# Optimization experiments

Hardware: AMD Instinct MI355X
Metric: run time of the kernel (lower is better)

## Reference

```python
import jax, jax.numpy as jnp
import numpy as np

D = 2048
N_SLOTS = 8
ALPHA_MIN = 0.02
FAST_DECAY = 0.95
ALPHA_BOOST = 1.0
B = 16384


def setup_inputs() -> dict:
    key = jax.random.key(0)
    ks = jax.random.split(key, 12)
    h = jax.random.normal(ks[0], (B, D), dtype=jnp.float32)
    neighbor_msg = jax.random.normal(ks[1], (B, D), dtype=jnp.float32)
    keys = jax.random.normal(ks[2], (N_SLOTS, D), dtype=jnp.float32) / (D ** 0.5)
    # torch nn.Linear convention: W [out, in], y = x @ W.T + b
    Wr = jax.random.normal(ks[3], (D, D), dtype=jnp.float32) * 0.02
    br = jnp.zeros((D,), dtype=jnp.float32)
    Wc = jax.random.normal(ks[4], (2, 2 * D), dtype=jnp.float32) * 0.02
    bc = jnp.zeros((2,), dtype=jnp.float32)
    Ww = jax.random.normal(ks[5], (D, 2 * D), dtype=jnp.float32) * 0.02
    bw = jnp.zeros((D,), dtype=jnp.float32)
    state = jax.random.normal(ks[6], (N_SLOTS, D), dtype=jnp.float32) * 0.1
    fast = jax.random.normal(ks[7], (N_SLOTS, D), dtype=jnp.float32) * 0.1
    return {"h": h, "neighbor_msg": neighbor_msg, "keys": keys,
            "Wr": Wr, "br": br, "Wc": Wc, "bc": bc, "Ww": Ww, "bw": bw,
            "state": state, "fast": fast}


def reference(h, neighbor_msg, keys, Wr, br, Wc, bc, Ww, bw, state, fast):
    # read_proj
    q = h @ Wr.T + br                                  # [B, D]
    attn = jax.nn.softmax(q @ keys.T, axis=-1)         # [B, n_slots]
    read = attn @ (state + fast)                       # [B, D]
    # ctrl -> add/erase gates (erase computed but unused downstream, as in source)
    ctrl = jnp.concatenate([h, read], axis=-1) @ Wc.T + bc   # [B, 2]
    add = jax.nn.sigmoid(ctrl[:, 0:1])
    erase = jax.nn.sigmoid(ctrl[:, 1:2])
    alpha = jnp.clip(ALPHA_MIN + (1.0 - ALPHA_MIN) * jnp.mean(add), 0.0, 1.0)
    alpha = jnp.clip(alpha * ALPHA_BOOST, 0.0, 1.0)
    # attention-weighted write into slots
    w_in = jnp.concatenate([h + neighbor_msg, read], axis=-1)  # [B, 2D]
    delta = attn.T @ (w_in @ Ww.T + bw)                # [n_slots, D]
    new_state = (1.0 - alpha) * state + alpha * delta
    new_fast = FAST_DECAY * fast + (1.0 - FAST_DECAY) * delta
    return read, attn, alpha, new_state, new_fast
```

## Files before the change

### kernel.cpp

```cpp
#include <hip/hip_runtime.h>
#include <math.h>

#define D 2048
#define NS 8
#define BTOT 16384

#define ATTN_OFF  ((size_t)BTOT * D)
#define ALPHA_OFF (ATTN_OFF + (size_t)BTOT * NS)
#define STATE_OFF (ALPHA_OFF + 1)
#define FAST_OFF  (STATE_OFF + (size_t)NS * D)

#define WS_SM    0
#define WS_KPX   16384
#define WS_GS    34816
#define WS_PB    51200
#define WS_LB    215040
#define WS_SWC   215048
#define WS_GALL  215056

__global__ void __launch_bounds__(256) kZ(const float* __restrict__ st, const float* __restrict__ fa,
                                          const float* __restrict__ Wc, float* __restrict__ ws) {
  int i = blockIdx.x * 256 + threadIdx.x;
  if (i < 16384) {
    ws[WS_SM + i] = st[i] + fa[i];
  } else if (i < 32768) {
    ws[WS_KPX + (i - 16384)] = 0.f;
  } else if (i < 34816) {
    ws[WS_KPX + 16384 + (i - 32768)] = Wc[i - 32768];
  } else if (i < 51200) {
    ws[WS_GS + (i - 34816)] = 0.f;
  } else if (i < 67584) {
    ws[WS_PB + (i - 51200)] = 0.f;
  } else if (i < 67680) {
    ws[WS_LB + (i - 67584)] = 0.f;
  }
}

__global__ void __launch_bounds__(256) kA(const float* __restrict__ keys,
                                          const float* __restrict__ Wr,
                                          float* __restrict__ kpx) {
  int e = blockIdx.x * 256 + threadIdx.x;
  int d0 = blockIdx.y * 64;
  float acc[NS] = {0.f,0.f,0.f,0.f,0.f,0.f,0.f,0.f};
  for (int d = d0; d < d0 + 64; ++d) {
    float wv = Wr[(size_t)d * D + e];
#pragma unroll
    for (int s = 0; s < NS; ++s) acc[s] += keys[s * D + d] * wv;
  }
#pragma unroll
  for (int s = 0; s < NS; ++s) atomicAdd(&kpx[s * D + e], acc[s]);
}

__global__ void __launch_bounds__(256) kC(const float* __restrict__ keys,
                                          const float* __restrict__ br,
                                          const float* __restrict__ Wc,
                                          const float* __restrict__ sm,
                                          float* __restrict__ lb, float* __restrict__ swc) {
  int t = threadIdx.x;
  int idx = blockIdx.x * 256 + t;
  float brv = br[idx];
  float wcr = Wc[D + idx];
  float v[16];
#pragma unroll
  for (int s = 0; s < NS; ++s) {
    v[s]     = keys[s * D + idx] * brv;
    v[8 + s] = sm[s * D + idx] * wcr;
  }
#pragma unroll
  for (int off = 32; off > 0; off >>= 1) {
#pragma unroll
    for (int k = 0; k < 16; ++k) v[k] += __shfl_down(v[k], off);
  }
  __shared__ float red[4 * 16];
  int lane = t & 63, wid = t >> 6;
  if (lane == 0) {
#pragma unroll
    for (int k = 0; k < 16; ++k) red[wid * 16 + k] = v[k];
  }
  __syncthreads();
  if (t < 16) {
    float tot = red[t] + red[16 + t] + red[32 + t] + red[48 + t];
    if (t < 8) atomicAdd(&lb[t], tot); else atomicAdd(&swc[t - 8], tot);
  }
}

__global__ void __launch_bounds__(256) k1aF(const float* __restrict__ h,
                                            const float* __restrict__ kpx,
                                            const float* __restrict__ lb, const float* __restrict__ swc,
                                            const float* __restrict__ bc,
                                            float* __restrict__ attn, float* __restrict__ gall) {
  __shared__ float4 kl[9 * 512];
  __shared__ float red2[4 * 9];
  int t = threadIdx.x;
  const float4* kp4 = (const float4*)kpx;
  for (int i = t; i < 4608; i += 256) kl[i] = kp4[i];
  __syncthreads();

  int w = t >> 6, lane = t & 63;
  int row0 = blockIdx.x * 32 + w * 8;
  float lbv[8], swv[8];
#pragma unroll
  for (int s = 0; s < NS; ++s) { lbv[s] = lb[s]; swv[s] = swc[s]; }
  float bc0 = bc[0];
  float cs[9] = {0.f,0.f,0.f,0.f,0.f,0.f,0.f,0.f,0.f};

  for (int r = 0; r < 8; ++r) {
    int row = row0 + r;
    const float4* h4 = (const float4*)h + (size_t)row * 512;
    float4 hv[8];
#pragma unroll
    for (int j = 0; j < 8; ++j) hv[j] = h4[lane + 64 * j];
    float acc[9] = {0.f,0.f,0.f,0.f,0.f,0.f,0.f,0.f,0.f};
#pragma unroll
    for (int j = 0; j < 8; ++j) {
#pragma unroll
      for (int s = 0; s < 9; ++s) {
        float4 kv = kl[s * 512 + lane + 64 * j];
        acc[s] += hv[j].x * kv.x + hv[j].y * kv.y + hv[j].z * kv.z + hv[j].w * kv.w;
      }
    }
#pragma unroll
    for (int off = 32; off > 0; off >>= 1) {
#pragma unroll
      for (int s = 0; s < 9; ++s) acc[s] += __shfl_xor(acc[s], off);
    }
    float lg[8]; float m = -1e30f;
#pragma unroll
    for (int s = 0; s < NS; ++s) { lg[s] = acc[s] + lbv[s]; m = fmaxf(m, lg[s]); }
    float sum = 0.f;
#pragma unroll
    for (int s = 0; s < NS; ++s) { lg[s] = expf(lg[s] - m); sum += lg[s]; }
    float inv = 1.f / sum;
    float x = acc[8] + bc0;
#pragma unroll
    for (int s = 0; s < NS; ++s) { lg[s] *= inv; x += lg[s] * swv[s]; cs[s] += lg[s]; }
    float add = 1.f / (1.f + expf(-x));
    cs[8] += add;
    if (lane == 0) {
      float4* ao = (float4*)(attn + (size_t)row * NS);
      ao[0] = make_float4(lg[0], lg[1], lg[2], lg[3]);
      ao[1] = make_float4(lg[4], lg[5], lg[6], lg[7]);
    }
  }
  if (lane == 0) {
#pragma unroll
    for (int k = 0; k < 9; ++k) red2[w * 9 + k] = cs[k];
  }
  __syncthreads();
  if (t < 9) {
    float tot = red2[t] + red2[9 + t] + red2[18 + t] + red2[27 + t];
    atomicAdd(&gall[64 + t], tot);
  }
}

static __device__ __forceinline__ float4 f4fma(float s, float4 a, float4 c) {
  c.x += s * a.x; c.y += s * a.y; c.z += s * a.z; c.w += s * a.w; return c;
}

__global__ void __launch_bounds__(256, 3) k2n(const float* __restrict__ h, const float* __restrict__ nm,
                                              const float* __restrict__ sm, const float* __restrict__ attn,
                                              float* __restrict__ readout, float* __restrict__ pb,
                                              float* __restrict__ gsb) {
  __shared__ float4 lp[4][NS][64];
  int t = threadIdx.x;
  int c4 = t & 63, r4 = t >> 6;
  int chunk = blockIdx.x, rc = blockIdx.y;
  int fbase = chunk * 64 + c4;
  const float4* sm4 = (const float4*)sm;
  float4 S[NS];
#pragma unroll
  for (int s = 0; s < NS; ++s) S[s] = sm4[s * 512 + fbase];
  float4 P[NS], Q[NS];
#pragma unroll
  for (int s = 0; s < NS; ++s) { P[s] = make_float4(0.f,0.f,0.f,0.f); Q[s] = make_float4(0.f,0.f,0.f,0.f); }
  int rowbase = rc * 128;
  for (int it = 0; it < 32; ++it) {
    int row = rowbase + it * 4 + r4;
    float4 hv = ((const float4*)h)[(size_t)row * 512 + fbase];
    float4 nv = ((const float4*)nm)[(size_t)row * 512 + fbase];
    const float* ar = attn + (size_t)row * NS;
    float a[NS];
#pragma unroll
    for (int s = 0; s < NS; ++s) a[s] = ar[s];
    float4 wv = make_float4(hv.x + nv.x, hv.y + nv.y, hv.z + nv.z, hv.w + nv.w);
    float4 rd = make_float4(0.f, 0.f, 0.f, 0.f);
#pragma unroll
    for (int s = 0; s < NS; ++s) {
      rd = f4fma(a[s], S[s], rd);
      P[s] = f4fma(a[s], wv, P[s]);
    }
#pragma unroll
    for (int s = 0; s < NS; ++s) Q[s] = f4fma(a[s], rd, Q[s]);
    ((float4*)readout)[(size_t)row * 512 + fbase] = rd;
  }
#pragma unroll
  for (int s = 0; s < NS; ++s) lp[r4][s][c4] = P[s];
  __syncthreads();
  for (int k = t; k < 512; k += 256) {
    int s = k >> 6, c = k & 63;
    float4 a0 = lp[0][s][c], b0 = lp[1][s][c], c0 = lp[2][s][c], d0 = lp[3][s][c];
    float4 v = make_float4(a0.x + b0.x + c0.x + d0.x, a0.y + b0.y + c0.y + d0.y,
                           a0.z + b0.z + c0.z + d0.z, a0.w + b0.w + c0.w + d0.w);
    float* dst = pb + s * D + chunk * 256 + c * 4;
    atomicAdd(dst + 0, v.x); atomicAdd(dst + 1, v.y);
    atomicAdd(dst + 2, v.z); atomicAdd(dst + 3, v.w);
  }
  __syncthreads();
#pragma unroll
  for (int s = 0; s < NS; ++s) lp[r4][s][c4] = Q[s];
  __syncthreads();
  for (int k = t; k < 512; k += 256) {
    int s = k >> 6, c = k & 63;
    float4 a0 = lp[0][s][c], b0 = lp[1][s][c], c0 = lp[2][s][c], d0 = lp[3][s][c];
    float4 v = make_float4(a0.x + b0.x + c0.x + d0.x, a0.y + b0.y + c0.y + d0.y,
                           a0.z + b0.z + c0.z + d0.z, a0.w + b0.w + c0.w + d0.w);
    float* dst = gsb + s * D + chunk * 256 + c * 4;
    atomicAdd(dst + 0, v.x); atomicAdd(dst + 1, v.y);
    atomicAdd(dst + 2, v.z); atomicAdd(dst + 3, v.w);
  }
}

__global__ void __launch_bounds__(256) k4(const float* __restrict__ Ww, const float* __restrict__ bw,
                                          const float* __restrict__ st, const float* __restrict__ fa,
                                          const float* __restrict__ p, const float* __restrict__ gs,
                                          const float* __restrict__ gall,
                                          float* __restrict__ outst, float* __restrict__ outfa,
                                          float* __restrict__ alphaout) {
  int dd = blockIdx.x, t = threadIdx.x;
  const float4* wr = (const float4*)(Ww + (size_t)dd * (2 * D));
  float4 w0 = wr[t], w1 = wr[256 + t], w2 = wr[512 + t], w3 = wr[768 + t];
  const float4* p4 = (const float4*)p;
  const float4* g4 = (const float4*)gs;
  float acc[NS];
#pragma unroll
  for (int s = 0; s < NS; ++s) {
    float4 pa = p4[s * 512 + t], pb2 = p4[s * 512 + 256 + t];
    float4 ga = g4[s * 512 + t], gb = g4[s * 512 + 256 + t];
    acc[s] = w0.x * pa.x + w0.y * pa.y + w0.z * pa.z + w0.w * pa.w
           + w1.x * pb2.x + w1.y * pb2.y + w1.z * pb2.z + w1.w * pb2.w
           + w2.x * ga.x + w2.y * ga.y + w2.z * ga.z + w2.w * ga.w
           + w3.x * gb.x + w3.y * gb.y + w3.z * gb.z + w3.w * gb.w;
  }
#pragma unroll
  for (int off = 32; off > 0; off >>= 1) {
#pragma unroll
    for (int v = 0; v < NS; ++v) acc[v] += __shfl_down(acc[v], off);
  }
  __shared__ float red[32];
  int lane = t & 63, wid = t >> 6;
  if (lane == 0) {
#pragma unroll
    for (int v = 0; v < NS; ++v) red[wid * 8 + v] = acc[v];
  }
  __syncthreads();
  if (t < NS) {
    float tot = red[t] + red[8 + t] + red[16 + t] + red[24 + t];
    float delta = tot + gall[64 + t] * bw[dd];
    float al = 0.02f + 0.98f * (gall[72] * (1.f / (float)BTOT));
    al = fminf(fmaxf(al, 0.f), 1.f);
    size_t idx = (size_t)t * D + dd;
    outst[idx] = (1.f - al) * st[idx] + al * delta;
    outfa[idx] = 0.95f * fa[idx] + 0.05f * delta;
  }
  if (dd == 0 && t == 0) {
    float al = 0.02f + 0.98f * (gall[72] * (1.f / (float)BTOT));
    alphaout[0] = fminf(fmaxf(al, 0.f), 1.f);
  }
}

extern "C" void kernel_launch(void* const* d_in, const int* in_sizes, int n_in,
                              void* d_out, int out_size, void* d_ws, size_t ws_size,
                              hipStream_t stream) {
  const float* h    = (const float*)d_in[0];
  const float* nm   = (const float*)d_in[1];
  const float* keys = (const float*)d_in[2];
  const float* Wr   = (const float*)d_in[3];
  const float* br   = (const float*)d_in[4];
  const float* Wc   = (const float*)d_in[5];
  const float* bc   = (const float*)d_in[6];
  const float* Ww   = (const float*)d_in[7];
  const float* bw   = (const float*)d_in[8];
  const float* st   = (const float*)d_in[9];
  const float* fa   = (const float*)d_in[10];
  float* out = (float*)d_out;
  float* ws  = (float*)d_ws;

  float* sm   = ws + WS_SM;
  float* kpx  = ws + WS_KPX;
  float* gsb  = ws + WS_GS;
  float* pb   = ws + WS_PB;
  float* lb   = ws + WS_LB;
  float* swc  = ws + WS_SWC;
  float* gall = ws + WS_GALL;
  float* attn = out + ATTN_OFF;

  kZ<<<265, 256, 0, stream>>>(st, fa, Wc, ws);
  kA<<<dim3(8, 32), 256, 0, stream>>>(keys, Wr, kpx);
  kC<<<8, 256, 0, stream>>>(keys, br, Wc, sm, lb, swc);
  k1aF<<<512, 256, 0, stream>>>(h, kpx, lb, swc, bc, attn, gall);
  k2n<<<dim3(8, 128), 256, 0, stream>>>(h, nm, sm, attn, out, pb, gsb);
  k4<<<2048, 256, 0, stream>>>(Ww, bw, st, fa, pb, gsb, gall, out + STATE_OFF, out + FAST_OFF,
                               out + ALPHA_OFF);
}
```

Before: 503.1 us.

## Replace attn^T·read accumulation with attention Gram matrix times slot memory

Since read = attn @ sm, the term attn^T @ read equals (attn^T attn) @ sm. The change drops the Q accumulation and second atomic pass in k2n and instead accumulates the 8x8 Gram matrix (36 upper entries) in the attention kernel. k4 then multiplies the Ww read-half against sm and combines with the Gram matrix. The attention kernel is also rewritten to use 16 threads per row reading kpx from global/L2 instead of LDS, and k2n is retiled to 32 columns by 8 row groups. This removes register pressure and half the atomics in k2n, at the cost of a 45-value shuffle reduction per row in k1r.

Result: faster. 444.5 us (-11.6%).

```diff
diff --git a/kernel.cpp b/kernel.cpp
--- a/kernel.cpp
+++ b/kernel.cpp
@@ -12,11 +12,10 @@
 
 #define WS_SM    0
 #define WS_KPX   16384
-#define WS_GS    34816
-#define WS_PB    51200
-#define WS_LB    215040
-#define WS_SWC   215048
-#define WS_GALL  215056
+#define WS_PB    34816
+#define WS_LB    51200
+#define WS_SWC   51208
+#define WS_GALL  51216
 
 __global__ void __launch_bounds__(256) kZ(const float* __restrict__ st, const float* __restrict__ fa,
                                           const float* __restrict__ Wc, float* __restrict__ ws) {
@@ -28,11 +27,9 @@
   } else if (i < 34816) {
     ws[WS_KPX + 16384 + (i - 32768)] = Wc[i - 32768];
   } else if (i < 51200) {
-    ws[WS_GS + (i - 34816)] = 0.f;
-  } else if (i < 67584) {
-    ws[WS_PB + (i - 51200)] = 0.f;
-  } else if (i < 67680) {
-    ws[WS_LB + (i - 67584)] = 0.f;
+    ws[WS_PB + (i - 34816)] = 0.f;
+  } else if (i < 51264) {
+    ws[WS_LB + (i - 51200)] = 0.f;
   }
 }
 
@@ -84,72 +81,70 @@
   }
 }
 
-__global__ void __launch_bounds__(256) k1aF(const float* __restrict__ h,
-                                            const float* __restrict__ kpx,
-                                            const float* __restrict__ lb, const float* __restrict__ swc,
-                                            const float* __restrict__ bc,
-                                            float* __restrict__ attn, float* __restrict__ gall) {
-  __shared__ float4 kl[9 * 512];
-  __shared__ float red2[4 * 9];
+__global__ void __launch_bounds__(256, 4) k1r(const float* __restrict__ h,
+                                              const float* __restrict__ kpx,
+                                              const float* __restrict__ lb, const float* __restrict__ swc,
+                                              const float* __restrict__ bc,
+                                              float* __restrict__ attn, float* __restrict__ gall) {
   int t = threadIdx.x;
+  int q = t & 15;
+  int row = blockIdx.x * 16 + (t >> 4);
+  const float4* h4 = (const float4*)h + (size_t)row * 512;
   const float4* kp4 = (const float4*)kpx;
-  for (int i = t; i < 4608; i += 256) kl[i] = kp4[i];
-  __syncthreads();
-
-  int w = t >> 6, lane = t & 63;
-  int row0 = blockIdx.x * 32 + w * 8;
-  float lbv[8], swv[8];
-#pragma unroll
-  for (int s = 0; s < NS; ++s) { lbv[s] = lb[s]; swv[s] = swc[s]; }
-  float bc0 = bc[0];
-  float cs[9] = {0.f,0.f,0.f,0.f,0.f,0.f,0.f,0.f,0.f};
-
-  for (int r = 0; r < 8; ++r) {
-    int row = row0 + r;
-    const float4* h4 = (const float4*)h + (size_t)row * 512;
-    float4 hv[8];
-#pragma unroll
-    for (int j = 0; j < 8; ++j) hv[j] = h4[lane + 64 * j];
-    float acc[9] = {0.f,0.f,0.f,0.f,0.f,0.f,0.f,0.f,0.f};
-#pragma unroll
-    for (int j = 0; j < 8; ++j) {
-#pragma unroll
-      for (int s = 0; s < 9; ++s) {
-        float4 kv = kl[s * 512 + lane + 64 * j];
-        acc[s] += hv[j].x * kv.x + hv[j].y * kv.y + hv[j].z * kv.z + hv[j].w * kv.w;
-      }
-    }
-#pragma unroll
-    for (int off = 32; off > 0; off >>= 1) {
-#pragma unroll
-      for (int s = 0; s < 9; ++s) acc[s] += __shfl_xor(acc[s], off);
-    }
-    float lg[8]; float m = -1e30f;
-#pragma unroll
-    for (int s = 0; s < NS; ++s) { lg[s] = acc[s] + lbv[s]; m = fmaxf(m, lg[s]); }
-    float sum = 0.f;
-#pragma unroll
-    for (int s = 0; s < NS; ++s) { lg[s] = expf(lg[s] - m); sum += lg[s]; }
-    float inv = 1.f / sum;
-    float x = acc[8] + bc0;
-#pragma unroll
-    for (int s = 0; s < NS; ++s) { lg[s] *= inv; x += lg[s] * swv[s]; cs[s] += lg[s]; }
-    float add = 1.f / (1.f + expf(-x));
-    cs[8] += add;
-    if (lane == 0) {
-      float4* ao = (float4*)(attn + (size_t)row * NS);
-      ao[0] = make_float4(lg[0], lg[1], lg[2], lg[3]);
-      ao[1] = make_float4(lg[4], lg[5], lg[6], lg[7]);
-    }
-  }
+  float acc[9] = {0.f,0.f,0.f,0.f,0.f,0.f,0.f,0.f,0.f};
+#pragma unroll 4
+  for (int j = 0; j < 32; ++j) {
+    float4 hv = h4[j * 16 + q];
+#pragma unroll
+    for (int s = 0; s < 9; ++s) {
+      float4 kv = kp4[s * 512 + j * 16 + q];
+      acc[s] += hv.x * kv.x + hv.y * kv.y + hv.z * kv.z + hv.w * kv.w;
+    }
+  }
+#pragma unroll
+  for (int off = 1; off <= 8; off <<= 1) {
+#pragma unroll
+    for (int s = 0; s < 9; ++s) acc[s] += __shfl_xor(acc[s], off);
+  }
+  float lg[8]; float m = -1e30f;
+#pragma unroll
+  for (int s = 0; s < NS; ++s) { lg[s] = acc[s] + lb[s]; m = fmaxf(m, lg[s]); }
+  float sum = 0.f;
+#pragma unroll
+  for (int s = 0; s < NS; ++s) { lg[s] = expf(lg[s] - m); sum += lg[s]; }
+  float inv = 1.f / sum;
+  float x = acc[8] + bc[0];
+#pragma unroll
+  for (int s = 0; s < NS; ++s) { lg[s] *= inv; x += lg[s] * swc[s]; }
+  float add = 1.f / (1.f + expf(-x));
+  if (q == 0) ((float4*)(attn + (size_t)row * NS))[0] = make_float4(lg[0], lg[1], lg[2], lg[3]);
+  if (q == 1) ((float4*)(attn + (size_t)row * NS))[1] = make_float4(lg[4], lg[5], lg[6], lg[7]);
+  float v[45];
+  {
+    int c = 0;
+#pragma unroll
+    for (int i = 0; i < NS; ++i)
+#pragma unroll
+      for (int j = i; j < NS; ++j) v[c++] = lg[i] * lg[j];
+  }
+#pragma unroll
+  for (int s = 0; s < NS; ++s) v[36 + s] = lg[s];
+  v[44] = add;
+#pragma unroll
+  for (int off = 16; off <= 32; off <<= 1) {
+#pragma unroll
+    for (int k = 0; k < 45; ++k) v[k] += __shfl_xor(v[k], off);
+  }
+  __shared__ float red[4][45];
+  int lane = t & 63, w = t >> 6;
   if (lane == 0) {
 #pragma unroll
-    for (int k = 0; k < 9; ++k) red2[w * 9 + k] = cs[k];
-  }
-  __syncthreads();
-  if (t < 9) {
-    float tot = red2[t] + red2[9 + t] + red2[18 + t] + red2[27 + t];
-    atomicAdd(&gall[64 + t], tot);
+    for (int k = 0; k < 45; ++k) red[w][k] = v[k];
+  }
+  __syncthreads();
+  if (t < 45) {
+    float tot = red[0][t] + red[1][t] + red[2][t] + red[3][t];
+    atomicAdd(&gall[t], tot);
   }
 }
 
@@ -157,25 +152,25 @@
   c.x += s * a.x; c.y += s * a.y; c.z += s * a.z; c.w += s * a.w; return c;
 }
 
-__global__ void __launch_bounds__(256, 3) k2n(const float* __restrict__ h, const float* __restrict__ nm,
+__global__ void __launch_bounds__(256, 4) k2n(const float* __restrict__ h, const float* __restrict__ nm,
                                               const float* __restrict__ sm, const float* __restrict__ attn,
-                                              float* __restrict__ readout, float* __restrict__ pb,
-                                              float* __restrict__ gsb) {
-  __shared__ float4 lp[4][NS][64];
+                                              float* __restrict__ readout, float* __restrict__ pb) {
+  __shared__ float4 lp[8][NS][32];
   int t = threadIdx.x;
-  int c4 = t & 63, r4 = t >> 6;
+  int c4 = t & 31, r4 = t >> 5;
   int chunk = blockIdx.x, rc = blockIdx.y;
-  int fbase = chunk * 64 + c4;
+  int fbase = chunk * 32 + c4;
   const float4* sm4 = (const float4*)sm;
   float4 S[NS];
 #pragma unroll
   for (int s = 0; s < NS; ++s) S[s] = sm4[s * 512 + fbase];
-  float4 P[NS], Q[NS];
-#pragma unroll
-  for (int s = 0; s < NS; ++s) { P[s] = make_float4(0.f,0.f,0.f,0.f); Q[s] = make_float4(0.f,0.f,0.f,0.f); }
-  int rowbase = rc * 128;
+  float4 P[NS];
+#pragma unroll
+  for (int s = 0; s < NS; ++s) P[s] = make_float4(0.f, 0.f, 0.f, 0.f);
+  int rowbase = rc * 256;
+#pragma unroll 2
   for (int it = 0; it < 32; ++it) {
-    int row = rowbase + it * 4 + r4;
+    int row = rowbase + it * 8 + r4;
     float4 hv = ((const float4*)h)[(size_t)row * 512 + fbase];
     float4 nv = ((const float4*)nm)[(size_t)row * 512 + fbase];
     const float* ar = attn + (size_t)row * NS;
@@ -189,40 +184,28 @@
       rd = f4fma(a[s], S[s], rd);
       P[s] = f4fma(a[s], wv, P[s]);
     }
-#pragma unroll
-    for (int s = 0; s < NS; ++s) Q[s] = f4fma(a[s], rd, Q[s]);
     ((float4*)readout)[(size_t)row * 512 + fbase] = rd;
   }
 #pragma unroll
   for (int s = 0; s < NS; ++s) lp[r4][s][c4] = P[s];
   __syncthreads();
-  for (int k = t; k < 512; k += 256) {
-    int s = k >> 6, c = k & 63;
-    float4 a0 = lp[0][s][c], b0 = lp[1][s][c], c0 = lp[2][s][c], d0 = lp[3][s][c];
-    float4 v = make_float4(a0.x + b0.x + c0.x + d0.x, a0.y + b0.y + c0.y + d0.y,
-                           a0.z + b0.z + c0.z + d0.z, a0.w + b0.w + c0.w + d0.w);
-    float* dst = pb + s * D + chunk * 256 + c * 4;
+  {
+    int s = t >> 5, c = t & 31;
+    float4 v = make_float4(0.f, 0.f, 0.f, 0.f);
+#pragma unroll
+    for (int g = 0; g < 8; ++g) {
+      float4 u = lp[g][s][c];
+      v.x += u.x; v.y += u.y; v.z += u.z; v.w += u.w;
+    }
+    float* dst = pb + s * D + chunk * 128 + c * 4;
     atomicAdd(dst + 0, v.x); atomicAdd(dst + 1, v.y);
     atomicAdd(dst + 2, v.z); atomicAdd(dst + 3, v.w);
   }
-  __syncthreads();
-#pragma unroll
-  for (int s = 0; s < NS; ++s) lp[r4][s][c4] = Q[s];
-  __syncthreads();
-  for (int k = t; k < 512; k += 256) {
-    int s = k >> 6, c = k & 63;
-    float4 a0 = lp[0][s][c], b0 = lp[1][s][c], c0 = lp[2][s][c], d0 = lp[3][s][c];
-    float4 v = make_float4(a0.x + b0.x + c0.x + d0.x, a0.y + b0.y + c0.y + d0.y,
-                           a0.z + b0.z + c0.z + d0.z, a0.w + b0.w + c0.w + d0.w);
-    float* dst = gsb + s * D + chunk * 256 + c * 4;
-    atomicAdd(dst + 0, v.x); atomicAdd(dst + 1, v.y);
-    atomicAdd(dst + 2, v.z); atomicAdd(dst + 3, v.w);
-  }
 }
 
 __global__ void __launch_bounds__(256) k4(const float* __restrict__ Ww, const float* __restrict__ bw,
                                           const float* __restrict__ st, const float* __restrict__ fa,
-                                          const float* __restrict__ p, const float* __restrict__ gs,
+                                          const float* __restrict__ p, const float* __restrict__ sm,
                                           const float* __restrict__ gall,
                                           float* __restrict__ outst, float* __restrict__ outfa,
                                           float* __restrict__ alphaout) {
@@ -230,40 +213,50 @@
   const float4* wr = (const float4*)(Ww + (size_t)dd * (2 * D));
   float4 w0 = wr[t], w1 = wr[256 + t], w2 = wr[512 + t], w3 = wr[768 + t];
   const float4* p4 = (const float4*)p;
-  const float4* g4 = (const float4*)gs;
-  float acc[NS];
+  const float4* s4 = (const float4*)sm;
+  float acc[16];
 #pragma unroll
   for (int s = 0; s < NS; ++s) {
     float4 pa = p4[s * 512 + t], pb2 = p4[s * 512 + 256 + t];
-    float4 ga = g4[s * 512 + t], gb = g4[s * 512 + 256 + t];
+    float4 sa = s4[s * 512 + t], sb = s4[s * 512 + 256 + t];
     acc[s] = w0.x * pa.x + w0.y * pa.y + w0.z * pa.z + w0.w * pa.w
-           + w1.x * pb2.x + w1.y * pb2.y + w1.z * pb2.z + w1.w * pb2.w
-           + w2.x * ga.x + w2.y * ga.y + w2.z * ga.z + w2.w * ga.w
-           + w3.x * gb.x + w3.y * gb.y + w3.z * gb.z + w3.w * gb.w;
+           + w1.x * pb2.x + w1.y * pb2.y + w1.z * pb2.z + w1.w * pb2.w;
+    acc[8 + s] = w2.x * sa.x + w2.y * sa.y + w2.z * sa.z + w2.w * sa.w
+               + w3.x * sb.x + w3.y * sb.y + w3.z * sb.z + w3.w * sb.w;
   }
 #pragma unroll
   for (int off = 32; off > 0; off >>= 1) {
 #pragma unroll
-    for (int v = 0; v < NS; ++v) acc[v] += __shfl_down(acc[v], off);
-  }
-  __shared__ float red[32];
+    for (int k = 0; k < 16; ++k) acc[k] += __shfl_down(acc[k], off);
+  }
+  __shared__ float red[4][16];
+  __shared__ float red2[16];
   int lane = t & 63, wid = t >> 6;
   if (lane == 0) {
 #pragma unroll
-    for (int v = 0; v < NS; ++v) red[wid * 8 + v] = acc[v];
-  }
+    for (int k = 0; k < 16; ++k) red[wid][k] = acc[k];
+  }
+  __syncthreads();
+  if (t < 16) red2[t] = red[0][t] + red[1][t] + red[2][t] + red[3][t];
   __syncthreads();
   if (t < NS) {
-    float tot = red[t] + red[8 + t] + red[16 + t] + red[24 + t];
-    float delta = tot + gall[64 + t] * bw[dd];
-    float al = 0.02f + 0.98f * (gall[72] * (1.f / (float)BTOT));
+    float delta = red2[t];
+#pragma unroll
+    for (int sp = 0; sp < NS; ++sp) {
+      int i = t < sp ? t : sp;
+      int j = t < sp ? sp : t;
+      int idx = i * 8 - (i * (i - 1)) / 2 + (j - i);
+      delta += gall[idx] * red2[8 + sp];
+    }
+    delta += gall[36 + t] * bw[dd];
+    float al = 0.02f + 0.98f * (gall[44] * (1.f / (float)BTOT));
     al = fminf(fmaxf(al, 0.f), 1.f);
-    size_t idx = (size_t)t * D + dd;
-    outst[idx] = (1.f - al) * st[idx] + al * delta;
-    outfa[idx] = 0.95f * fa[idx] + 0.05f * delta;
+    size_t idx2 = (size_t)t * D + dd;
+    outst[idx2] = (1.f - al) * st[idx2] + al * delta;
+    outfa[idx2] = 0.95f * fa[idx2] + 0.05f * delta;
   }
   if (dd == 0 && t == 0) {
-    float al = 0.02f + 0.98f * (gall[72] * (1.f / (float)BTOT));
+    float al = 0.02f + 0.98f * (gall[44] * (1.f / (float)BTOT));
     alphaout[0] = fminf(fmaxf(al, 0.f), 1.f);
   }
 }
@@ -287,18 +280,17 @@
 
   float* sm   = ws + WS_SM;
   float* kpx  = ws + WS_KPX;
-  float* gsb  = ws + WS_GS;
   float* pb   = ws + WS_PB;
   float* lb   = ws + WS_LB;
   float* swc  = ws + WS_SWC;
   float* gall = ws + WS_GALL;
   float* attn = out + ATTN_OFF;
 
-  kZ<<<265, 256, 0, stream>>>(st, fa, Wc, ws);
+  kZ<<<201, 256, 0, stream>>>(st, fa, Wc, ws);
   kA<<<dim3(8, 32), 256, 0, stream>>>(keys, Wr, kpx);
   kC<<<8, 256, 0, stream>>>(keys, br, Wc, sm, lb, swc);
-  k1aF<<<512, 256, 0, stream>>>(h, kpx, lb, swc, bc, attn, gall);
-  k2n<<<dim3(8, 128), 256, 0, stream>>>(h, nm, sm, attn, out, pb, gsb);
-  k4<<<2048, 256, 0, stream>>>(Ww, bw, st, fa, pb, gsb, gall, out + STATE_OFF, out + FAST_OFF,
+  k1r<<<1024, 256, 0, stream>>>(h, kpx, lb, swc, bc, attn, gall);
+  k2n<<<dim3(16, 64), 256, 0, stream>>>(h, nm, sm, attn, out, pb);
+  k4<<<2048, 256, 0, stream>>>(Ww, bw, st, fa, pb, sm, gall, out + STATE_OFF, out + FAST_OFF,
                                out + ALPHA_OFF);
 }
```
